# Kernel tuning notes

Hardware: AMD Instinct MI355X
Metric: run time of the kernel (lower is better)

Reference implementation:

```python
import jax, jax.numpy as jnp
import numpy as np

R = 4                 # correlation radius
D = 2 * R + 1         # window size per axis (9)
EPS = 1e-5            # batchnorm eps
DN = ('NCHW', 'OIHW', 'NCHW')


def conv(x, w, stride=1, pad=1):
    return jax.lax.conv_general_dilated(x, w, (stride, stride), [(pad, pad), (pad, pad)], dimension_numbers=DN)


def bn(x, g, b):
    # training-mode batchnorm (batch statistics over N,H,W), matching torch default
    m = jnp.mean(x, axis=(0, 2, 3), keepdims=True)
    v = jnp.var(x, axis=(0, 2, 3), keepdims=True)
    return g[None, :, None, None] * (x - m) * jax.lax.rsqrt(v + EPS) + b[None, :, None, None]


def grid_sample(img, grid):
    # bilinear, align_corners=True, zero padding; img (B,C,H,W), grid (B,Ho,Wo,2) in [-1,1]
    B, C, H, W = img.shape
    x = (grid[..., 0] + 1.0) * (W - 1) * 0.5
    y = (grid[..., 1] + 1.0) * (H - 1) * 0.5
    x0 = jnp.floor(x)
    y0 = jnp.floor(y)

    def gather(xi, yi):
        valid = (xi >= 0) & (xi <= W - 1) & (yi >= 0) & (yi <= H - 1)
        xc = jnp.clip(xi, 0, W - 1).astype(jnp.int32)
        yc = jnp.clip(yi, 0, H - 1).astype(jnp.int32)
        v = jax.vmap(lambda im, yy, xx: im[:, yy, xx])(img, yc, xc)  # (B,C,Ho,Wo)
        return v * valid[:, None, :, :].astype(img.dtype)

    wx1 = (x - x0)[:, None]; wx0 = 1.0 - wx1
    wy1 = (y - y0)[:, None]; wy0 = 1.0 - wy1
    return (wy0 * wx0 * gather(x0, y0) + wy0 * wx1 * gather(x0 + 1.0, y0)
            + wy1 * wx0 * gather(x0, y0 + 1.0) + wy1 * wx1 * gather(x0 + 1.0, y0 + 1.0))


def _forward(f1, f2, coords, w1, g1, b1, w2, g2, b2, w3, g3, b3, w4, g4, b4,
             wd, gd, bd, w5, b5, e1w, e1b, e2w, e2b, e3w, e3b, dapw):
    B, C, H, W = f1.shape
    dx = jnp.linspace(-R, R, D)
    delta = jnp.stack(jnp.meshgrid(dx, dx, indexing='ij'), axis=-1)      # (D,D,2)

    # sampling centroids for the (2r+1)^2 displacement window
    cp = coords.transpose(0, 2, 3, 1)                                     # (B,H,W,2)
    cent = cp[:, None, :, None, :, :] + delta.reshape(1, D, 1, D, 1, 2)   # (B,D,H,D,W,2)
    gx = 2.0 * cent[..., 0] / (W - 1) - 1.0
    gy = 2.0 * cent[..., 1] / (H - 1) - 1.0
    grid = jnp.stack([gx, gy], axis=-1).reshape(B, D * H, D * W, 2)

    f2s = grid_sample(f2, grid).reshape(B, C, D, H, D, W).transpose(0, 2, 4, 1, 3, 5)  # (B,D,D,C,H,W)
    f1s = jnp.broadcast_to(f1[:, None, None], (B, D, D, C, H, W))
    ds = jnp.broadcast_to(delta.reshape(1, D, D, 2, 1, 1), (B, D, D, 2, H, W)).astype(f1.dtype)
    stack = jnp.concatenate([f1s, f2s, ds], axis=3).reshape(B * D * D, 2 * C + 2, H, W)

    # MatchingNet (DICL-style): conv/bn/relu with stride-2 down + transposed-conv up
    x = jax.nn.relu(bn(conv(stack, w1), g1, b1))
    x = jax.nn.relu(bn(conv(x, w2, stride=2), g2, b2))
    x = jax.nn.relu(bn(conv(x, w3), g3, b3))
    x = jax.nn.relu(bn(conv(x, w4), g4, b4))
    # ConvTranspose2d(k=4, s=2, p=1) == dilated conv with lhs_dilation=2, pad=k-1-p=2
    x = jax.lax.conv_general_dilated(x, wd, (1, 1), [(2, 2), (2, 2)], lhs_dilation=(2, 2), dimension_numbers=DN)
    x = jax.nn.relu(bn(x, gd, bd))
    cost = (conv(x, w5) + b5[None, :, None, None]).reshape(B, D * D, H, W)

    # PairEmbedding: 1x1-conv MLP on the same stacked volume
    e = jax.nn.relu(conv(stack, e1w, pad=0) + e1b[None, :, None, None])
    e = jax.nn.relu(conv(e, e2w, pad=0) + e2b[None, :, None, None])
    e = (conv(e, e3w, pad=0) + e3b[None, :, None, None]).reshape(B, D * D, -1, H, W)

    # DAP (1x1 conv over displacement channels) + windowed softmax-weighted reduction
    score = jax.nn.softmax(jnp.einsum('od,bdhw->bohw', dapw, cost), axis=1)
    emb = jnp.sum(score[:, :, None] * e, axis=1)                           # (B,emb_dim,H,W)
    return jnp.concatenate([cost, emb], axis=1)                            # (B,81+32,H,W)


def setup_inputs() -> dict:
    keys = iter(jax.random.split(jax.random.key(0), 40))
    B, C, H, W = 2, 32, 64, 64
    cin = 2 * C + 2

    def p(shape, fan):
        return jax.random.normal(next(keys), shape, jnp.float32) * np.float32(np.sqrt(2.0 / fan))

    f1 = jax.random.normal(next(keys), (B, C, H, W), jnp.float32)
    f2 = jax.random.normal(next(keys), (B, C, H, W), jnp.float32)
    yy, xx = jnp.meshgrid(jnp.arange(H, dtype=jnp.float32), jnp.arange(W, dtype=jnp.float32), indexing='ij')
    base = jnp.stack([xx, yy], axis=0)[None]                               # pixel grid (x,y)
    coords = base + 4.0 * jax.random.normal(next(keys), (B, 2, H, W), jnp.float32)

    inp = dict(f1=f1, f2=f2, coords=coords)
    inp.update(w1=p((96, cin, 3, 3), cin * 9), g1=jnp.ones(96), b1=jnp.zeros(96))
    inp.update(w2=p((128, 96, 3, 3), 96 * 9), g2=jnp.ones(128), b2=jnp.zeros(128))
    inp.update(w3=p((128, 128, 3, 3), 128 * 9), g3=jnp.ones(128), b3=jnp.zeros(128))
    inp.update(w4=p((64, 128, 3, 3), 128 * 9), g4=jnp.ones(64), b4=jnp.zeros(64))
    inp.update(wd=p((32, 64, 4, 4), 64 * 16), gd=jnp.ones(32), bd=jnp.zeros(32))
    inp.update(w5=p((1, 32, 3, 3), 32 * 9), b5=jnp.zeros(1))
    inp.update(e1w=p((48, cin, 1, 1), cin), e1b=jnp.zeros(48))
    inp.update(e2w=p((64, 48, 1, 1), 48), e2b=jnp.zeros(64))
    inp.update(e3w=p((32, 64, 1, 1), 64), e3b=jnp.zeros(32))
    inp.update(dapw=jnp.eye(D * D, dtype=jnp.float32))
    return inp


def reference(f1, f2, coords, w1, g1, b1, w2, g2, b2, w3, g3, b3, w4, g4, b4,
              wd, gd, bd, w5, b5, e1w, e1b, e2w, e2b, e3w, e3b, dapw):
    return _forward(f1, f2, coords, w1, g1, b1, w2, g2, b2, w3, g3, b3, w4, g4, b4,
                    wd, gd, bd, w5, b5, e1w, e1b, e2w, e2b, e3w, e3b, dapw)
```

## Files before the change

### kernel.cpp

```cpp
#include <hip/hip_runtime.h>
#include <hip/hip_bf16.h>

typedef _Float16 hf;
typedef short    s8v  __attribute__((ext_vector_type(8)));
typedef _Float16 h8v  __attribute__((ext_vector_type(8)));
typedef float    f32x4 __attribute__((ext_vector_type(4)));

#define DEVINL __device__ __forceinline__

DEVINL unsigned short f2h_bits(float f) { return __builtin_bit_cast(unsigned short, (hf)f); }
DEVINL float h2f_bits(unsigned short u) { return (float)__builtin_bit_cast(hf, u); }

static constexpr size_t OFF_SA    = 0;
static constexpr size_t OFF_F2S   = 524288;
static constexpr size_t OFF_E1    = 42991616;
static constexpr size_t OFF_E2    = 106692608;
static constexpr size_t OFF_E3    = 42991616;
static constexpr size_t OFF_X1    = 85458944;
static constexpr size_t OFF_X2    = 524288;
static constexpr size_t OFF_X3    = 85458944;
static constexpr size_t OFF_X4    = 524288;
static constexpr size_t OFF_XD    = 127926272;
static constexpr size_t OFF_SCORE = 524288;
static constexpr size_t OFF_STATS = 212860928;
static constexpr size_t OFF_WC1   = 212871168;
static constexpr size_t OFF_WC2   = 212981760;
static constexpr size_t OFF_WC3   = 213202944;
static constexpr size_t OFF_WC4   = 213497856;
static constexpr size_t OFF_WDC   = 213645312;
static constexpr size_t OFF_WE1   = 213720064;
static constexpr size_t OFF_WE2   = 213726208;
static constexpr size_t OFF_WE3   = 213734400;
static constexpr size_t OFF_DT1   = 213738496;
static constexpr size_t OFF_DTE   = 213745408;
static constexpr size_t OFF_F2CLF = 213746048;

__global__ void prepack(const float* __restrict__ src, hf* __restrict__ dst,
                        int COr, int COP, int CINr, int CINsrc, int KP, int TAPS) {
  const int idx = blockIdx.x * 256 + threadIdx.x;
  const int total = TAPS * COP * KP;
  if (idx >= total) return;
  const int k = idx % KP;
  const int r = idx / KP;
  const int co = r % COP;
  const int t = r / COP;
  float v = 0.f;
  if (co < COr && k < CINr) v = src[((size_t)co * CINsrc + k) * TAPS + t];
  dst[idx] = (hf)v;
}

__global__ void prepack2(const float* __restrict__ src, hf* __restrict__ dst,
                         int COP, int CIN, int NCHn) {
  const int idx = blockIdx.x * 256 + threadIdx.x;
  const int total = 9 * NCHn * COP * 32;
  if (idx >= total) return;
  const int kk = idx & 31;
  const int r = idx >> 5;
  const int co = r % COP;
  const int r2 = r / COP;
  const int ks = r2 % NCHn;
  const int t = r2 / NCHn;
  dst[idx] = (hf)src[((size_t)co * CIN + ks * 32 + kk) * 9 + t];
}

__global__ void prepack2d(const float* __restrict__ src, hf* __restrict__ dst) {
  const int idx = blockIdx.x * 256 + threadIdx.x;
  if (idx >= 32768) return;
  const int kk = idx & 31;
  const int co = (idx >> 5) & 31;
  const int ks = (idx >> 10) & 1;
  const int tt = (idx >> 11) & 3;
  const int par = idx >> 13;
  const int qq = par >> 1, pp = par & 1;
  const int a = tt >> 1, b = tt & 1;
  dst[idx] = (hf)src[(((size_t)co * 64 + ks * 32 + kk) * 4 + (qq + 2 * a)) * 4 + (pp + 2 * b)];
}

__global__ void dtab1_kernel(const float* __restrict__ w1, float* __restrict__ dtab) {
  const int idx = blockIdx.x * 256 + threadIdx.x;
  if (idx >= 96 * 9 * 2) return;
  const int c = idx & 1;
  const int r = idx >> 1;
  const int pat = r % 9;
  const int co = r / 9;
  const int rc = pat / 3, cc = pat % 3;
  const int kh0 = (rc == 0) ? 1 : 0, kh1 = (rc == 2) ? 1 : 2;
  const int kw0 = (cc == 0) ? 1 : 0, kw1 = (cc == 2) ? 1 : 2;
  float s = 0.f;
  for (int kh = kh0; kh <= kh1; ++kh)
    for (int kw = kw0; kw <= kw1; ++kw)
      s += w1[((size_t)(co * 66 + 64 + c) * 3 + kh) * 3 + kw];
  dtab[(co * 9 + pat) * 2 + c] = s;
}

__global__ void dtabE_kernel(const float* __restrict__ e1w, float* __restrict__ dtE) {
  const int co = threadIdx.x;
  if (co < 48) {
    dtE[co * 2 + 0] = e1w[co * 66 + 64];
    dtE[co * 2 + 1] = e1w[co * 66 + 65];
  }
}

__global__ __launch_bounds__(256) void packf1(const float* __restrict__ f1, hf* __restrict__ sA) {
  const int gid = blockIdx.x * 256 + threadIdx.x;
  const int b = gid >> 12, pix = gid & 4095;
  unsigned words[16];
#pragma unroll
  for (int c = 0; c < 32; c += 2) {
    const float v0 = f1[((size_t)(b * 32 + c)) * 4096 + pix];
    const float v1 = f1[((size_t)(b * 32 + c + 1)) * 4096 + pix];
    words[c >> 1] = (unsigned)f2h_bits(v0) | ((unsigned)f2h_bits(v1) << 16);
  }
  uint4* dst = (uint4*)(sA + (size_t)gid * 32);
#pragma unroll
  for (int i = 0; i < 4; ++i)
    dst[i] = make_uint4(words[4 * i], words[4 * i + 1], words[4 * i + 2], words[4 * i + 3]);
}

__global__ __launch_bounds__(256) void packf2f32(const float* __restrict__ f2,
                                                 float* __restrict__ dst) {
  const int gid = blockIdx.x * 256 + threadIdx.x;
  const int b = gid >> 12, pix = gid & 4095;
  float* op = dst + (size_t)gid * 32;
#pragma unroll
  for (int c = 0; c < 32; c += 4) {
    float4 v;
    v.x = f2[((size_t)(b * 32 + c + 0)) * 4096 + pix];
    v.y = f2[((size_t)(b * 32 + c + 1)) * 4096 + pix];
    v.z = f2[((size_t)(b * 32 + c + 2)) * 4096 + pix];
    v.w = f2[((size_t)(b * 32 + c + 3)) * 4096 + pix];
    *(float4*)(op + c) = v;
  }
}

__global__ __launch_bounds__(256) void sample2(const float* __restrict__ f2clf,
                                               const float* __restrict__ coords,
                                               hf* __restrict__ f2s) {
  const int gid = blockIdx.x * 256 + threadIdx.x;
  const int n = gid >> 12, pix = gid & 4095;
  const int b = n / 81, ij = n - b * 81;
  const float di = (float)(ij / 9) - 4.f, dj = (float)(ij % 9) - 4.f;
  const float x = coords[((size_t)(b * 2 + 0)) * 4096 + pix] + di;
  const float y = coords[((size_t)(b * 2 + 1)) * 4096 + pix] + dj;
  const float x0f = floorf(x), y0f = floorf(y);
  const int x0 = (int)x0f, y0 = (int)y0f;
  const float wx1 = x - x0f, wx0 = 1.f - wx1;
  const float wy1 = y - y0f, wy0 = 1.f - wy1;
  const bool vx0 = (unsigned)x0 < 64u, vx1 = (unsigned)(x0 + 1) < 64u;
  const bool vy0 = (unsigned)y0 < 64u, vy1 = (unsigned)(y0 + 1) < 64u;
  const int x0c = min(max(x0, 0), 63), x1c = min(max(x0 + 1, 0), 63);
  const int y0c = min(max(y0, 0), 63), y1c = min(max(y0 + 1, 0), 63);
  const float w00 = (vy0 && vx0) ? wy0 * wx0 : 0.f;
  const float w01 = (vy0 && vx1) ? wy0 * wx1 : 0.f;
  const float w10 = (vy1 && vx0) ? wy1 * wx0 : 0.f;
  const float w11 = (vy1 && vx1) ? wy1 * wx1 : 0.f;
  const float* fb = f2clf + (size_t)b * 4096 * 32;
  const float* p00 = fb + (size_t)(y0c * 64 + x0c) * 32;
  const float* p01 = fb + (size_t)(y0c * 64 + x1c) * 32;
  const float* p10 = fb + (size_t)(y1c * 64 + x0c) * 32;
  const float* p11 = fb + (size_t)(y1c * 64 + x1c) * 32;
  unsigned words[16];
#pragma unroll
  for (int ch = 0; ch < 16; ++ch) {
    const float2 a  = *(const float2*)(p00 + ch * 2);
    const float2 bb = *(const float2*)(p01 + ch * 2);
    const float2 c  = *(const float2*)(p10 + ch * 2);
    const float2 d  = *(const float2*)(p11 + ch * 2);
    const float v0 = w00 * a.x + w01 * bb.x + w10 * c.x + w11 * d.x;
    const float v1 = w00 * a.y + w01 * bb.y + w10 * c.y + w11 * d.y;
    words[ch] = (unsigned)f2h_bits(v0) | ((unsigned)f2h_bits(v1) << 16);
  }
  uint4* dst = (uint4*)(f2s + (size_t)gid * 32);
#pragma unroll
  for (int i = 0; i < 4; ++i)
    dst[i] = make_uint4(words[4 * i], words[4 * i + 1], words[4 * i + 2], words[4 * i + 3]);
}

DEVINL s8v bnin_apply(s8v v, const float* bnst, int gci) {
  const f32x4 scA = *(const f32x4*)(bnst + 256 + gci);
  const f32x4 scB = *(const f32x4*)(bnst + 256 + gci + 4);
  const f32x4 shA = *(const f32x4*)(bnst + 384 + gci);
  const f32x4 shB = *(const f32x4*)(bnst + 384 + gci + 4);
  h8v h = __builtin_bit_cast(h8v, v);
#pragma unroll
  for (int jj = 0; jj < 8; ++jj) {
    const float sc = (jj < 4) ? scA[jj] : scB[jj - 4];
    const float sh = (jj < 4) ? shA[jj] : shB[jj - 4];
    h[jj] = (hf)fmaxf((float)h[jj] * sc + sh, 0.f);
// ... 58 lines not shown
          const int gci = k0 + lg * 8;
          if (gci < G)
            bfr = *(const h8v*)(src1 + (((size_t)n * NPIXI + pix) * G + gci));
        }
#pragma unroll
        for (int mf = 0; mf < MFR; ++mf)
          acc[mf][pf] = __builtin_amdgcn_mfma_f32_16x16x32_f16(afr[mf], bfr, acc[mf][pf], 0, 0, 0);
      }
    }
  } else {
    s8v rbuf[CPT];
    auto stage_load = [&](int k0) {
#pragma unroll
      for (int j = 0; j < CPT; ++j) {
        const int cidx = tid + j * 256;
        s8v v = (s8v){0, 0, 0, 0, 0, 0, 0, 0};
        if (cidx < NCHUNK) {
          const int s = cidx >> 2, p = cidx & 3;
          const int rs = s / TC, cs = s - rs * TC;
          int ir, ic;
          if (GEOM == 1) { ir = 2 * r0 - 1 + rs; ic = (cs < 32) ? 2 * cs : 2 * (cs - 32) - 1; }
          else           { ir = r0 - 1 + rs;     ic = cs - 1; }
          const int gci = k0 + p * 8;
          if (((unsigned)ir < (unsigned)IMGI) && ((unsigned)ic < (unsigned)IMGI)) {
            const int ipix = ir * IMGI + ic;
            if (DUAL) {
              if (gci < 32)
                v = *(const s8v*)(src0 + (((size_t)b * NPIXI + ipix) * 32 + gci));
              else
                v = *(const s8v*)(src1 + (((size_t)n * NPIXI + ipix) * 32 + (gci - 32)));
            } else if (gci < G) {
              v = *(const s8v*)(src1 + (((size_t)n * NPIXI + ipix) * G + gci));
              if constexpr (BNIN) v = bnin_apply(v, bnst, gci);
            }
          }
        }
        rbuf[j] = v;
      }
    };
    auto stage_write = [&]() {
#pragma unroll
      for (int j = 0; j < CPT; ++j) {
        const int cidx = tid + j * 256;
        if (cidx < NCHUNK) {
          const int s = cidx >> 2, p = cidx & 3;
          *(s8v*)(&lds[(size_t)(p * PSTR + s) * 8]) = rbuf[j];
        }
      }
    };

    stage_load(0);
#pragma unroll
    for (int ch = 0; ch < NCH; ++ch) {
      if (ch > 0) __syncthreads();
      stage_write();
      __syncthreads();
      if (ch + 1 < NCH) stage_load((ch + 1) * 32);
      const int k0 = ch * 32;
#pragma unroll
      for (int t = 0; t < TAPS; ++t) {
        int dh, dw, wt, kh = 0, kw = 0;
        if (GEOM == 2) {
          dh = qq + (t >> 1) - 1; dw = pp + (t & 1) - 1;
          wt = (qq + 2 * (t >> 1)) * 4 + (pp + 2 * (t & 1));
        } else { kh = t / 3; kw = t % 3; dh = kh - 1; dw = kw - 1; wt = t; }
        h8v afr[MFR];
#pragma unroll
        for (int mf = 0; mf < MFR; ++mf)
          afr[mf] = *(const h8v*)(wp + ((size_t)(wt * COP + co0 + mf * 16 + ln)) * KP + k0 + lg * 8);
#pragma unroll
        for (int pf = 0; pf < WPIX; ++pf) {
          const int pl = wid * (WPIX * 16) + pf * 16 + ln;
          const int rL = pl / IMGO, c = pl - rL * IMGO;
          int slot;
          if (GEOM == 1) slot = (2 * rL + kh) * 65 + ((kw == 1) ? c : (32 + c + (kw >> 1)));
          else           slot = (rL + dh + 1) * TC + (c + dw + 1);
          const h8v bfr = *(const h8v*)(&lds[(size_t)(lg * PSTR + slot) * 8]);
#pragma unroll
          for (int mf = 0; mf < MFR; ++mf)
            acc[mf][pf] = __builtin_amdgcn_mfma_f32_16x16x32_f16(afr[mf], bfr, acc[mf][pf], 0, 0, 0);
        }
      }
    }
  }

  const float di = (float)(ij / 9) - 4.f, dj = (float)(ij % 9) - 4.f;

  {
#pragma unroll
    for (int mf = 0; mf < MFR; ++mf) {
#pragma unroll
      for (int pf = 0; pf < WPIX; ++pf) {
        const int pl = wid * (WPIX * 16) + pf * 16 + ln;
        const int rL = pl / IMGO, c = pl - rL * IMGO;
        int opix;
        if constexpr (GEOM == 2) opix = (2 * (r0 + rL) + qq) * 64 + 2 * c + pp;
        else opix = (r0 + rL) * IMGO + c;
        if constexpr (DELTA && EPI == 0) {
          const int oh = r0 + rL;
          const int rc = (oh == 0) ? 0 : ((oh == IMGO - 1) ? 2 : 1);
          const int cc = (c == 0) ? 0 : ((c == IMGO - 1) ? 2 : 1);
#pragma unroll
          for (int rg = 0; rg < 4; ++rg) {
            const int co = co0 + mf * 16 + lg * 4 + rg;
            acc[mf][pf][rg] += di * dtab[(co * 9 + rc * 3 + cc) * 2 + 0] +
                               dj * dtab[(co * 9 + rc * 3 + cc) * 2 + 1];
          }
        }
        if constexpr (DELTA && EPI == 1) {
#pragma unroll
          for (int rg = 0; rg < 4; ++rg) {
            const int co = co0 + mf * 16 + lg * 4 + rg;
            acc[mf][pf][rg] += di * dtab[co * 2] + dj * dtab[co * 2 + 1];
          }
        }
        if constexpr (EPI == 1 || EPI == 2) {
          const float4 bv = *(const float4*)(bias + co0 + mf * 16 + lg * 4);
          acc[mf][pf][0] += bv.x; acc[mf][pf][1] += bv.y;
          acc[mf][pf][2] += bv.z; acc[mf][pf][3] += bv.w;
          if constexpr (EPI == 1) {
#pragma unroll
            for (int rg = 0; rg < 4; ++rg) acc[mf][pf][rg] = fmaxf(acc[mf][pf][rg], 0.f);
          }
        }
        ushort4 st;
        st.x = f2h_bits(acc[mf][pf][0]); st.y = f2h_bits(acc[mf][pf][1]);
        st.z = f2h_bits(acc[mf][pf][2]); st.w = f2h_bits(acc[mf][pf][3]);
        *reinterpret_cast<ushort4*>(outB + ((size_t)n * NPIXO + opix) * COB + co0 + mf * 16 + lg * 4) = st;
      }
    }
    if constexpr (EPI == 0) {
      __syncthreads();
      float* sl = (float*)lds;
#pragma unroll
      for (int mf = 0; mf < MFR; ++mf) {
#pragma unroll
        for (int rg = 0; rg < 4; ++rg) {
          float s = 0.f, q2 = 0.f;
#pragma unroll
          for (int pf = 0; pf < WPIX; ++pf) {
            const float v = acc[mf][pf][rg];
            s += v; q2 += v * v;
          }
#pragma unroll
          for (int o = 1; o < 16; o <<= 1) { s += __shfl_xor(s, o); q2 += __shfl_xor(q2, o); }
          if (ln == 0) {
            const int cl = mf * 16 + lg * 4 + rg;
            sl[(wid * MFR * 16 + cl) * 2 + 0] = s;
            sl[(wid * MFR * 16 + cl) * 2 + 1] = q2;
          }
        }
      }
      __syncthreads();
      for (int i = tid; i < MFR * 16 * 2; i += 256) {
        const int cl = i >> 1, stt = i & 1;
        float tot = 0.f;
#pragma unroll
        for (int w = 0; w < 4; ++w) tot += sl[(w * MFR * 16 + cl) * 2 + stt];
        atomicAdd(&statL[2 * (co0 + cl) + stt], tot);
      }
    }
  }
  (void)outF;
}

__global__ __launch_bounds__(256) void mconv2s2(
    const hf* __restrict__ src1, const hf* __restrict__ wp,
    const float* __restrict__ bnst, float* __restrict__ statL, hf* __restrict__ outB) {
  constexpr int IMGI = 64, IMGO = 32;
  constexpr int PIXROWS = 4, WPIX = 2, MFR = 4;
  constexpr int TR = 2 * PIXROWS + 1;
  constexpr int TC = 65;
  constexpr int NSLOT = TR * TC;
  constexpr int PSTR = NSLOT + 1;
  constexpr int NCH = 3;
  constexpr int G = 96;
  constexpr int NPIXI = IMGI * IMGI;
  constexpr int NCHUNK = NSLOT * 4;
  constexpr int COT = MFR * 16;
  constexpr int COP = 128;
  constexpr int WPLANE = 3 * COT;
  constexpr int WPSTR  = WPLANE + 1;
  constexpr int WCHUNK = WPLANE * 4;

  __shared__ __align__(16) hf alds[4 * PSTR * 8];
  __shared__ __align__(16) hf wlds[4 * WPSTR * 8];

  const int tid = threadIdx.x;
  const int wid = tid >> 6, lane = tid & 63, lg = lane >> 4, ln = lane & 15;
  const int n = blockIdx.z;
  const int r0 = blockIdx.x * PIXROWS;
  const int co0 = (int)blockIdx.y * COT;

  f32x4 acc[MFR][WPIX];
#pragma unroll
  for (int mf = 0; mf < MFR; ++mf)
#pragma unroll
    for (int pf = 0; pf < WPIX; ++pf) acc[mf][pf] = (f32x4){0.f, 0.f, 0.f, 0.f};

  for (int ks = 0; ks < NCH; ++ks) {
    const int k0 = ks * 32;
    __syncthreads();
    for (int cidx = tid; cidx < NCHUNK; cidx += 256) {
      const int s = cidx >> 2, p = cidx & 3;
      const int rs = s / TC, cs = s - rs * TC;
      const int ir = 2 * r0 - 1 + rs;
      const int ic = (cs < 32) ? 2 * cs : 2 * (cs - 32) - 1;
      s8v v = (s8v){0, 0, 0, 0, 0, 0, 0, 0};
      const int gci = k0 + p * 8;
      if (((unsigned)ir < (unsigned)IMGI) && ((unsigned)ic < (unsigned)IMGI)) {
        const int ipix = ir * IMGI + ic;
        v = *(const s8v*)(src1 + (((size_t)n * NPIXI + ipix) * G + gci));
        v = bnin_apply(v, bnst, gci);
      }
      *(s8v*)(&alds[(size_t)(p * PSTR + s) * 8]) = v;
    }
#pragma unroll
    for (int tg = 0; tg < 3; ++tg) {
      if (tg > 0) __syncthreads();
      for (int widx = tid; widx < WCHUNK; widx += 256) {
        const int p = widx & 3;
        const int r = widx >> 2;
        const int co = r & (COT - 1);
        const int tt = r >> 6;
        const int tglob = tg * 3 + tt;
        const s8v wv = *(const s8v*)(wp + (((size_t)(tglob * NCH + ks) * COP + co0 + co) * 32 + p * 8));
        *(s8v*)(&wlds[(size_t)(p * WPSTR + r) * 8]) = wv;
      }
      __syncthreads();
#pragma unroll
      for (int tt = 0; tt < 3; ++tt) {
        const int kh = tg, kw = tt;
        h8v afr[MFR];
#pragma unroll
        for (int mf = 0; mf < MFR; ++mf)
          afr[mf] = *(const h8v*)(&wlds[(size_t)(lg * WPSTR + tt * COT + mf * 16 + ln) * 8]);
#pragma unroll
        for (int pf = 0; pf < WPIX; ++pf) {
          const int pl = wid * (WPIX * 16) + pf * 16 + ln;
          const int rL = pl / IMGO, c = pl - rL * IMGO;
          const int slot = (2 * rL + kh) * 65 + ((kw == 1) ? c : (32 + c + (kw >> 1)));
          const h8v bfr = *(const h8v*)(&alds[(size_t)(lg * PSTR + slot) * 8]);
#pragma unroll
          for (int mf = 0; mf < MFR; ++mf)
            acc[mf][pf] = __builtin_amdgcn_mfma_f32_16x16x32_f16(afr[mf], bfr, acc[mf][pf], 0, 0, 0);
        }
      }
    }
  }

#pragma unroll
  for (int mf = 0; mf < MFR; ++mf) {
#pragma unroll
    for (int pf = 0; pf < WPIX; ++pf) {
      const int pl = wid * (WPIX * 16) + pf * 16 + ln;
      const int rL = pl / IMGO, c = pl - rL * IMGO;
      const int opix = (r0 + rL) * IMGO + c;
      ushort4 st;
      st.x = f2h_bits(acc[mf][pf][0]); st.y = f2h_bits(acc[mf][pf][1]);
      st.z = f2h_bits(acc[mf][pf][2]); st.w = f2h_bits(acc[mf][pf][3]);
      *reinterpret_cast<ushort4*>(outB + ((size_t)n * 1024 + opix) * COP + co0 + mf * 16 + lg * 4) = st;
    }
  }
  __syncthreads();
  float* sl = (float*)alds;
#pragma unroll
  for (int mf = 0; mf < MFR; ++mf) {
#pragma unroll
    for (int rg = 0; rg < 4; ++rg) {
      float s = 0.f, q2 = 0.f;
#pragma unroll
      for (int pf = 0; pf < WPIX; ++pf) {
        const float v = acc[mf][pf][rg];
        s += v; q2 += v * v;
      }
#pragma unroll
      for (int o = 1; o < 16; o <<= 1) { s += __shfl_xor(s, o); q2 += __shfl_xor(q2, o); }
      if (ln == 0) {
        const int cl = mf * 16 + lg * 4 + rg;
        sl[(wid * MFR * 16 + cl) * 2 + 0] = s;
        sl[(wid * MFR * 16 + cl) * 2 + 1] = q2;
      }
    }
  }
  __syncthreads();
  for (int i = tid; i < MFR * 16 * 2; i += 256) {
    const int cl = i >> 1, stt = i & 1;
    float tot = 0.f;
#pragma unroll
    for (int w = 0; w < 4; ++w) tot += sl[(w * MFR * 16 + cl) * 2 + stt];
    atomicAdd(&statL[2 * (co0 + cl) + stt], tot);
  }
}

template <int G, int COP, int MFR, int PIXROWS, int WPIX, bool BNIN>
__global__ __launch_bounds__(256) void mconv2(
    const hf* __restrict__ src1, const hf* __restrict__ wp,
    const float* __restrict__ bnst,
    float* __restrict__ statL, hf* __restrict__ outB) {
  constexpr int IMG = 32;
  constexpr int TAPS = 9;
  constexpr int TC = IMG + 2;
  constexpr int TR = PIXROWS + 2;
  constexpr int NSLOT = TR * TC;
  constexpr int PSTR = NSLOT + 1;
  constexpr int NCH = G / 32;
  constexpr int NPIX = IMG * IMG;
  constexpr int NCHUNK = NSLOT * 4;
  constexpr int COT = MFR * 16;
  constexpr int WPLANE = TAPS * COT;
  constexpr int WPSTR  = WPLANE + 1;
  constexpr int WCHUNK = WPLANE * 4;

  __shared__ __align__(16) hf alds[4 * PSTR * 8];
  __shared__ __align__(16) hf wlds[4 * WPSTR * 8];

  const int tid = threadIdx.x;
  const int wid = tid >> 6, lane = tid & 63, lg = lane >> 4, ln = lane & 15;
  const int n = blockIdx.z;
  const int r0 = blockIdx.x * PIXROWS;
  const int co0 = blockIdx.y * COT;

  f32x4 acc[MFR][WPIX];
#pragma unroll
  for (int mf = 0; mf < MFR; ++mf)
#pragma unroll
    for (int pf = 0; pf < WPIX; ++pf) acc[mf][pf] = (f32x4){0.f, 0.f, 0.f, 0.f};

  for (int ks = 0; ks < NCH; ++ks) {
    __syncthreads();
    for (int cidx = tid; cidx < NCHUNK; cidx += 256) {
      const int s = cidx >> 2, p = cidx & 3;
      const int rs = s / TC, cs = s - rs * TC;
      const int ir = r0 - 1 + rs, ic = cs - 1;
      s8v v = (s8v){0, 0, 0, 0, 0, 0, 0, 0};
      if (((unsigned)ir < (unsigned)IMG) && ((unsigned)ic < (unsigned)IMG)) {
        const int ipix = ir * IMG + ic;
        v = *(const s8v*)(src1 + (((size_t)n * NPIX + ipix) * G + ks * 32 + p * 8));
        if constexpr (BNIN) v = bnin_apply(v, bnst, ks * 32 + p * 8);
      }
      *(s8v*)(&alds[(size_t)(p * PSTR + s) * 8]) = v;
    }
    for (int widx = tid; widx < WCHUNK; widx += 256) {
      const int p = widx & 3;
      const int r = widx >> 2;
      const int co = r & (COT - 1);
      const int t = r >> 6;
      const s8v wv = *(const s8v*)(wp + (((size_t)(t * NCH + ks) * COP + co0 + co) * 32 + p * 8));
      *(s8v*)(&wlds[(size_t)(p * WPSTR + r) * 8]) = wv;
    }
    __syncthreads();
#pragma unroll
    for (int t = 0; t < TAPS; ++t) {
      const int kh = t / 3, kw = t % 3;
      const int dh = kh - 1, dw = kw - 1;
      h8v afr[MFR];
#pragma unroll
      for (int mf = 0; mf < MFR; ++mf)
        afr[mf] = *(const h8v*)(&wlds[(size_t)(lg * WPSTR + t * COT + mf * 16 + ln) * 8]);
#pragma unroll
      for (int pf = 0; pf < WPIX; ++pf) {
        const int pl = wid * (WPIX * 16) + pf * 16 + ln;
        const int rL = pl / IMG, c = pl - rL * IMG;
        const int slot = (rL + dh + 1) * TC + (c + dw + 1);
        const h8v bfr = *(const h8v*)(&alds[(size_t)(lg * PSTR + slot) * 8]);
#pragma unroll
        for (int mf = 0; mf < MFR; ++mf)
          acc[mf][pf] = __builtin_amdgcn_mfma_f32_16x16x32_f16(afr[mf], bfr, acc[mf][pf], 0, 0, 0);
      }
    }
  }

#pragma unroll
  for (int mf = 0; mf < MFR; ++mf) {
#pragma unroll
    for (int pf = 0; pf < WPIX; ++pf) {
      const int pl = wid * (WPIX * 16) + pf * 16 + ln;
      const int rL = pl / IMG, c = pl - rL * IMG;
      const int opix = (r0 + rL) * IMG + c;
      ushort4 st;
      st.x = f2h_bits(acc[mf][pf][0]); st.y = f2h_bits(acc[mf][pf][1]);
      st.z = f2h_bits(acc[mf][pf][2]); st.w = f2h_bits(acc[mf][pf][3]);
      *reinterpret_cast<ushort4*>(outB + ((size_t)n * NPIX + opix) * COP + co0 + mf * 16 + lg * 4) = st;
    }
  }
  __syncthreads();
  float* sl = (float*)alds;
#pragma unroll
  for (int mf = 0; mf < MFR; ++mf) {
#pragma unroll
    for (int rg = 0; rg < 4; ++rg) {
      float s = 0.f, q2 = 0.f;
#pragma unroll
      for (int pf = 0; pf < WPIX; ++pf) {
        const float v = acc[mf][pf][rg];
        s += v; q2 += v * v;
      }
#pragma unroll
      for (int o = 1; o < 16; o <<= 1) { s += __shfl_xor(s, o); q2 += __shfl_xor(q2, o); }
      if (ln == 0) {
        const int cl = mf * 16 + lg * 4 + rg;
        sl[(wid * MFR * 16 + cl) * 2 + 0] = s;
        sl[(wid * MFR * 16 + cl) * 2 + 1] = q2;
      }
    }
  }
  __syncthreads();
  for (int i = tid; i < MFR * 16 * 2; i += 256) {
    const int cl = i >> 1, stt = i & 1;
    float tot = 0.f;
#pragma unroll
    for (int w = 0; w < 4; ++w) tot += sl[(w * MFR * 16 + cl) * 2 + stt];
    atomicAdd(&statL[2 * (co0 + cl) + stt], tot);
  }
}

__global__ __launch_bounds__(256) void mconv2d(
    const hf* __restrict__ src1, const hf* __restrict__ wp,
    const float* __restrict__ bnst,
    float* __restrict__ statL, hf* __restrict__ outB) {
  constexpr int IMG = 32;
  constexpr int TAPS = 4;
  constexpr int PIXROWS = 8;
  constexpr int WPIX = 4;
  constexpr int MFR = 2;
  constexpr int TC = IMG + 2;
  constexpr int TR = PIXROWS + 2;
  constexpr int NSLOT = TR * TC;
  constexpr int PSTR = NSLOT + 1;
  constexpr int NCH = 2;
  constexpr int NPIX = IMG * IMG;
  constexpr int NCHUNK = NSLOT * 4;
  constexpr int COT = MFR * 16;
  constexpr int WPLANE = TAPS * COT;
  constexpr int WPSTR  = WPLANE + 1;
  constexpr int WCHUNK = WPLANE * 4;
  constexpr int G = 64;

  __shared__ __align__(16) hf alds[4 * PSTR * 8];
  __shared__ __align__(16) hf wlds[4 * WPSTR * 8];

  const int tid = threadIdx.x;
  const int wid = tid >> 6, lane = tid & 63, lg = lane >> 4, ln = lane & 15;
  const int n = blockIdx.z;
  const int r0 = blockIdx.x * PIXROWS;
  const int par = blockIdx.y;
  const int qq = par >> 1, pp = par & 1;
  const hf* wbase = wp + (size_t)par * (TAPS * NCH * COT * 32);

  f32x4 acc[MFR][WPIX];
#pragma unroll
  for (int mf = 0; mf < MFR; ++mf)
#pragma unroll
    for (int pf = 0; pf < WPIX; ++pf) acc[mf][pf] = (f32x4){0.f, 0.f, 0.f, 0.f};

  for (int ks = 0; ks < NCH; ++ks) {
    __syncthreads();
    const int k0 = ks * 32;
    for (int cidx = tid; cidx < NCHUNK; cidx += 256) {
      const int s = cidx >> 2, p = cidx & 3;
      const int rs = s / TC, cs = s - rs * TC;
      const int ir = r0 - 1 + rs, ic = cs - 1;
      s8v v = (s8v){0, 0, 0, 0, 0, 0, 0, 0};
      if (((unsigned)ir < (unsigned)IMG) && ((unsigned)ic < (unsigned)IMG)) {
        const int ipix = ir * IMG + ic;
        v = *(const s8v*)(src1 + (((size_t)n * NPIX + ipix) * G + k0 + p * 8));
        v = bnin_apply(v, bnst, k0 + p * 8);
      }
      *(s8v*)(&alds[(size_t)(p * PSTR + s) * 8]) = v;
    }
    for (int widx = tid; widx < WCHUNK; widx += 256) {
      const int p = widx & 3;
      const int r = widx >> 2;
      const int co = r & (COT - 1);
      const int t = r >> 5;
      const s8v wv = *(const s8v*)(wbase + (((size_t)(t * NCH + ks) * COT + co) * 32 + p * 8));
      *(s8v*)(&wlds[(size_t)(p * WPSTR + r) * 8]) = wv;
    }
    __syncthreads();
#pragma unroll
    for (int t = 0; t < TAPS; ++t) {
      const int dh = qq + (t >> 1) - 1;
      const int dw = pp + (t & 1) - 1;
      h8v afr[MFR];
#pragma unroll
      for (int mf = 0; mf < MFR; ++mf)
        afr[mf] = *(const h8v*)(&wlds[(size_t)(lg * WPSTR + t * COT + mf * 16 + ln) * 8]);
#pragma unroll
      for (int pf = 0; pf < WPIX; ++pf) {
        const int pl = wid * (WPIX * 16) + pf * 16 + ln;
        const int rL = pl / IMG, c = pl - rL * IMG;
        const int slot = (rL + dh + 1) * TC + (c + dw + 1);
        const h8v bfr = *(const h8v*)(&alds[(size_t)(lg * PSTR + slot) * 8]);
#pragma unroll
        for (int mf = 0; mf < MFR; ++mf)
          acc[mf][pf] = __builtin_amdgcn_mfma_f32_16x16x32_f16(afr[mf], bfr, acc[mf][pf], 0, 0, 0);
      }
    }
  }

#pragma unroll
  for (int mf = 0; mf < MFR; ++mf) {
#pragma unroll
    for (int pf = 0; pf < WPIX; ++pf) {
      const int pl = wid * (WPIX * 16) + pf * 16 + ln;
      const int rL = pl / IMG, c = pl - rL * IMG;
      const int opix = (2 * (r0 + rL) + qq) * 64 + 2 * c + pp;
      ushort4 st;
      st.x = f2h_bits(acc[mf][pf][0]); st.y = f2h_bits(acc[mf][pf][1]);
      st.z = f2h_bits(acc[mf][pf][2]); st.w = f2h_bits(acc[mf][pf][3]);
      *reinterpret_cast<ushort4*>(outB + ((size_t)n * 4096 + opix) * 32 + mf * 16 + lg * 4) = st;
    }
  }
  __syncthreads();
  float* sl = (float*)alds;
#pragma unroll
  for (int mf = 0; mf < MFR; ++mf) {
#pragma unroll
    for (int rg = 0; rg < 4; ++rg) {
      float s = 0.f, q2 = 0.f;
#pragma unroll
      for (int pf = 0; pf < WPIX; ++pf) {
        const float v = acc[mf][pf][rg];
        s += v; q2 += v * v;
      }
#pragma unroll
      for (int o = 1; o < 16; o <<= 1) { s += __shfl_xor(s, o); q2 += __shfl_xor(q2, o); }
      if (ln == 0) {
        const int cl = mf * 16 + lg * 4 + rg;
        sl[(wid * MFR * 16 + cl) * 2 + 0] = s;
        sl[(wid * MFR * 16 + cl) * 2 + 1] = q2;
      }
    }
  }
  __syncthreads();
  for (int i = tid; i < MFR * 16 * 2; i += 256) {
    const int cl = i >> 1, stt = i & 1;
    float tot = 0.f;
#pragma unroll
    for (int w = 0; w < 4; ++w) tot += sl[(w * MFR * 16 + cl) * 2 + stt];
    atomicAdd(&statL[2 * cl + stt], tot);
  }
}

__global__ void bnfin_kernel(float* __restrict__ statL, const float* __restrict__ g,
                             const float* __restrict__ bt, int C, float invCnt) {
  const int c = threadIdx.x;
  if (c < C) {
    const float m = statL[2 * c] * invCnt;
    const float var = statL[2 * c + 1] * invCnt - m * m;
    const float sc = g[c] * rsqrtf(var + 1e-5f);
    statL[256 + c] = sc;
    statL[384 + c] = bt[c] - m * sc;
  }
}

__global__ __launch_bounds__(256) void conv5_kernel(
    const hf* __restrict__ xd, const float* __restrict__ w5, const float* __restrict__ b5,
    const float* __restrict__ bnst, float* __restrict__ outp) {
  const int gid = blockIdx.x * 256 + threadIdx.x;
  const int n = gid >> 12, pix = gid & 4095;
  const int b = n / 81, ij = n - b * 81;
  const int oh = pix >> 6, ow = pix & 63;
  float acc = b5[0];
#pragma unroll
  for (int kh = 0; kh < 3; ++kh) {
    const int ih = oh + kh - 1;
#pragma unroll
    for (int kw = 0; kw < 3; ++kw) {
      const int iw = ow + kw - 1;
      if (((unsigned)ih < 64u) && ((unsigned)iw < 64u)) {
        const hf* xp = xd + ((size_t)n * 4096 + ih * 64 + iw) * 32;
#pragma unroll
        for (int cq = 0; cq < 4; ++cq) {
          const h8v v = *(const h8v*)(xp + cq * 8);
#pragma unroll
          for (int j = 0; j < 8; ++j) {
            const int c = cq * 8 + j;
            const float t = (hf)fmaxf((float)v[j] * bnst[256 + c] + bnst[384 + c], 0.f);
            acc += t * w5[c * 9 + kh * 3 + kw];
          }
        }
      }
    }
  }
  outp[((size_t)(b * 113 + ij)) * 4096 + pix] = acc;
}

__global__ __launch_bounds__(64) void softmax_kernel(
    const float* __restrict__ outp, const float* __restrict__ dapw, float* __restrict__ score) {
  __shared__ float cb[64 * 81];
  __shared__ float sb[64 * 81];
  const int t = threadIdx.x;
  const int gid = blockIdx.x * 64 + t;
  const int b = gid >> 12, hw = gid & 4095;
  for (int d = 0; d < 81; ++d)
    cb[t * 81 + d] = outp[((size_t)(b * 113 + d)) * 4096 + hw];
  float smax = -1e30f;
  for (int o = 0; o < 81; ++o) {
    float s = 0.f;
    const float* dr = dapw + o * 81;
    for (int d = 0; d < 81; ++d) s += dr[d] * cb[t * 81 + d];
    sb[t * 81 + o] = s;
    smax = fmaxf(smax, s);
  }
  float sum = 0.f;
  for (int o = 0; o < 81; ++o) {
    const float e = __expf(sb[t * 81 + o] - smax);
    sb[t * 81 + o] = e;
    sum += e;
  }
  const float inv = 1.f / sum;
  for (int o = 0; o < 81; ++o)
    score[((size_t)(b * 81 + o)) * 4096 + hw] = sb[t * 81 + o] * inv;
}

__global__ __launch_bounds__(256) void emb_kernel(
    const float* __restrict__ score, const hf* __restrict__ e3, float* __restrict__ outp) {
  const int idx = blockIdx.x * 256 + threadIdx.x;
  const int b = idx >> 17, r = idx & 131071, m = r >> 12, hw = r & 4095;
  float acc = 0.f;
  for (int d = 0; d < 81; ++d) {
    const float sc = score[((size_t)(b * 81 + d)) * 4096 + hw];
    acc += sc * (float)e3[(((size_t)(b * 81 + d)) * 4096 + hw) * 32 + m];
  }
  outp[((size_t)(b * 113 + 81 + m)) * 4096 + hw] = acc;
}

extern "C" void kernel_launch(void* const* d_in, const int* in_sizes, int n_in,
                              void* d_out, int out_size, void* d_ws, size_t ws_size,
                              hipStream_t stream) {
  const float* f1     = (const float*)d_in[0];
  const float* f2     = (const float*)d_in[1];
  const float* coords = (const float*)d_in[2];
  const float* w1     = (const float*)d_in[3];
  const float* g1     = (const float*)d_in[4];
  const float* bb1    = (const float*)d_in[5];
  const float* w2     = (const float*)d_in[6];
  const float* g2     = (const float*)d_in[7];
  const float* bb2    = (const float*)d_in[8];
  const float* w3     = (const float*)d_in[9];
  const float* g3     = (const float*)d_in[10];
  const float* bb3    = (const float*)d_in[11];
  const float* w4     = (const float*)d_in[12];
  const float* g4     = (const float*)d_in[13];
  const float* bb4    = (const float*)d_in[14];
  const float* wdcv   = (const float*)d_in[15];
  const float* gd     = (const float*)d_in[16];
  const float* bbd    = (const float*)d_in[17];
  const float* w5     = (const float*)d_in[18];
  const float* b5     = (const float*)d_in[19];
  const float* e1w    = (const float*)d_in[20];
  const float* e1bi   = (const float*)d_in[21];
  const float* e2w    = (const float*)d_in[22];
  const float* e2bi   = (const float*)d_in[23];
  const float* e3w    = (const float*)d_in[24];
  const float* e3bi   = (const float*)d_in[25];
  const float* dapw   = (const float*)d_in[26];
  float* out = (float*)d_out;
  char* ws = (char*)d_ws;

  hf* sA  = (hf*)(ws + OFF_SA);
  hf* f2s = (hf*)(ws + OFF_F2S);
  hf* be1 = (hf*)(ws + OFF_E1);
  hf* be2 = (hf*)(ws + OFF_E2);
  hf* be3 = (hf*)(ws + OFF_E3);
  hf* x1  = (hf*)(ws + OFF_X1);
  hf* x2  = (hf*)(ws + OFF_X2);
  hf* x3  = (hf*)(ws + OFF_X3);
  hf* x4  = (hf*)(ws + OFF_X4);
  hf* xd  = (hf*)(ws + OFF_XD);
  float* score = (float*)(ws + OFF_SCORE);
  float* stats = (float*)(ws + OFF_STATS);
  hf* wc1 = (hf*)(ws + OFF_WC1);
  hf* wc2 = (hf*)(ws + OFF_WC2);
  hf* wc3 = (hf*)(ws + OFF_WC3);
  hf* wc4 = (hf*)(ws + OFF_WC4);
  hf* wdc = (hf*)(ws + OFF_WDC);
  hf* we1 = (hf*)(ws + OFF_WE1);
  hf* we2 = (hf*)(ws + OFF_WE2);
  hf* we3 = (hf*)(ws + OFF_WE3);
  float* dt1 = (float*)(ws + OFF_DT1);
  float* dtE = (float*)(ws + OFF_DTE);
  float* f2clf = (float*)(ws + OFF_F2CLF);

  hipMemsetAsync(stats, 0, 2560 * sizeof(float), stream);

  prepack<<<216, 256, 0, stream>>>(w1,   wc1, 96, 96, 64, 66, 64, 9);
  prepack2<<<432, 256, 0, stream>>>(w2,  wc2, 128, 96, 3);
  prepack2<<<576, 256, 0, stream>>>(w3,  wc3, 128, 128, 4);
  prepack2<<<288, 256, 0, stream>>>(w4,  wc4, 64, 128, 4);
  prepack2d<<<128, 256, 0, stream>>>(wdcv, wdc);
  prepack<<<12,  256, 0, stream>>>(e1w,  we1, 48, 48, 64, 66, 64, 1);
  prepack<<<16,  256, 0, stream>>>(e2w,  we2, 64, 64, 48, 48, 64, 1);
  prepack<<<8,   256, 0, stream>>>(e3w,  we3, 32, 32, 64, 64, 64, 1);
  dtab1_kernel<<<7, 256, 0, stream>>>(w1, dt1);
  dtabE_kernel<<<1, 96, 0, stream>>>(e1w, dtE);

  packf1<<<32, 256, 0, stream>>>(f1, sA);
  packf2f32<<<32, 256, 0, stream>>>(f2, f2clf);
  sample2<<<2592, 256, 0, stream>>>(f2clf, coords, f2s);

  mconv<3, 1, true, false, 32, 64, 48, 48, 3, 64, 64, 4, 4, true>
      <<<dim3(16, 1, 162), 256, 0, stream>>>(f2s, sA, we1, e1bi, dtE, nullptr, nullptr, be1, nullptr);
  mconv<3, 1, false, false, 48, 64, 64, 64, 4, 64, 64, 4, 4, false>
      <<<dim3(16, 1, 162), 256, 0, stream>>>(be1, nullptr, we2, e2bi, nullptr, nullptr, nullptr, be2, nullptr);
  mconv<3, 2, false, false, 64, 64, 32, 32, 2, 64, 64, 4, 4, false>
      <<<dim3(16, 1, 162), 256, 0, stream>>>(be2, nullptr, we3, e3bi, nullptr, nullptr, nullptr, be3, nullptr);

  mconv<0, 0, true, false, 32, 64, 96, 96, 3, 64, 64, 4, 4, true>
      <<<dim3(16, 2, 162), 256, 0, stream>>>(f2s, sA, wc1, nullptr, dt1, stats + 0, nullptr, x1, nullptr);
  bnfin_kernel<<<1, 128, 0, stream>>>(stats + 0, g1, bb1, 96, 1.f / 663552.f);

  mconv2s2<<<dim3(8, 2, 162), 256, 0, stream>>>(x1, wc2, stats + 0, stats + 512, x2);
  bnfin_kernel<<<1, 128, 0, stream>>>(stats + 512, g2, bb2, 128, 1.f / 165888.f);

  mconv2<128, 128, 4, 4, 2, true>
      <<<dim3(8, 2, 162), 256, 0, stream>>>(x2, wc3, stats + 512, stats + 1024, x3);
  bnfin_kernel<<<1, 128, 0, stream>>>(stats + 1024, g3, bb3, 128, 1.f / 165888.f);

  mconv2<128, 64, 4, 4, 2, true>
      <<<dim3(8, 1, 162), 256, 0, stream>>>(x3, wc4, stats + 1024, stats + 1536, x4);
  bnfin_kernel<<<1, 128, 0, stream>>>(stats + 1536, g4, bb4, 64, 1.f / 165888.f);

  mconv2d<<<dim3(4, 4, 162), 256, 0, stream>>>(x4, wdc, stats + 1536, stats + 2048, xd);
  bnfin_kernel<<<1, 128, 0, stream>>>(stats + 2048, gd, bbd, 32, 1.f / 663552.f);

  conv5_kernel<<<2592, 256, 0, stream>>>(xd, w5, b5, stats + 2048, out);

  softmax_kernel<<<128, 64, 0, stream>>>(out, dapw, score);
  emb_kernel<<<1024, 256, 0, stream>>>(score, be3, out);

  (void)in_sizes; (void)n_in; (void)out_size; (void)ws_size;
}
```

Measured before the change: 924.9 us.

## Fuse embedding 1x1 conv chain and replace BN-stat atomics with partial-sum reduction

Three 1x1 embedding conv kernels become one kernel that keeps the intermediate activations in LDS, so the be1/be2 buffers no longer go through global memory. BatchNorm statistics are no longer accumulated with float atomicAdd. Each block writes its partial sums to a per-block slot, a new bnred kernel reduces them in double precision, and bnfin computes scale and shift in double. This removes atomic contention and the extra round trips to global memory, at the cost of a few more small launches, and it also changes numerical precision and determinism.

```diff
diff --git a/kernel.cpp b/kernel.cpp
--- a/kernel.cpp
+++ b/kernel.cpp
@@ -13,8 +13,6 @@
 
 static constexpr size_t OFF_SA    = 0;
 static constexpr size_t OFF_F2S   = 524288;
-static constexpr size_t OFF_E1    = 42991616;
-static constexpr size_t OFF_E2    = 106692608;
 static constexpr size_t OFF_E3    = 42991616;
 static constexpr size_t OFF_X1    = 85458944;
 static constexpr size_t OFF_X2    = 524288;
@@ -34,6 +32,8 @@
 static constexpr size_t OFF_DT1   = 213738496;
 static constexpr size_t OFF_DTE   = 213745408;
 static constexpr size_t OFF_F2CLF = 213746048;
+static constexpr size_t OFF_PART  = 214794752;
+static constexpr size_t OFF_STATD = 216785920;
 
 __global__ void prepack(const float* __restrict__ src, hf* __restrict__ dst,
                         int COr, int COP, int CINr, int CINsrc, int KP, int TAPS) {
@@ -398,16 +398,158 @@
         }
       }
       __syncthreads();
+      const int NPB = gridDim.x * gridDim.z;
+      const int pb = (int)blockIdx.x * gridDim.z + blockIdx.z;
       for (int i = tid; i < MFR * 16 * 2; i += 256) {
         const int cl = i >> 1, stt = i & 1;
         float tot = 0.f;
 #pragma unroll
         for (int w = 0; w < 4; ++w) tot += sl[(w * MFR * 16 + cl) * 2 + stt];
-        atomicAdd(&statL[2 * (co0 + cl) + stt], tot);
+        statL[(size_t)((co0 + cl) * 2 + stt) * NPB + pb] = tot;
       }
     }
   }
   (void)outF;
+}
+
+__global__ __launch_bounds__(256) void efuse(
+    const hf* __restrict__ f2s_, const hf* __restrict__ sA_,
+    const hf* __restrict__ w1p, const float* __restrict__ b1v, const float* __restrict__ dtE,
+    const hf* __restrict__ w2p, const float* __restrict__ b2v,
+    const hf* __restrict__ w3p, const float* __restrict__ b3v,
+    hf* __restrict__ outB) {
+  constexpr int PSTRE = 72;
+  __shared__ __align__(16) hf ldsA[256 * PSTRE];
+  __shared__ __align__(16) hf ldsB[256 * PSTRE];
+
+  const int tid = threadIdx.x;
+  const int wid = tid >> 6, lane = tid & 63, lg = lane >> 4, ln = lane & 15;
+  const int n = blockIdx.z, b = n / 81, ij = n - b * 81;
+  const int r0 = blockIdx.x * 4;
+  const float di = (float)(ij / 9) - 4.f, dj = (float)(ij % 9) - 4.f;
+
+  f32x4 acc1[3][4];
+#pragma unroll
+  for (int mf = 0; mf < 3; ++mf)
+#pragma unroll
+    for (int pf = 0; pf < 4; ++pf) acc1[mf][pf] = (f32x4){0.f, 0.f, 0.f, 0.f};
+#pragma unroll
+  for (int ch = 0; ch < 2; ++ch) {
+    const int k0 = ch * 32;
+    h8v afr[3];
+#pragma unroll
+    for (int mf = 0; mf < 3; ++mf)
+      afr[mf] = *(const h8v*)(w1p + ((size_t)(mf * 16 + ln)) * 64 + k0 + lg * 8);
+#pragma unroll
+    for (int pf = 0; pf < 4; ++pf) {
+      const int pix = r0 * 64 + wid * 64 + pf * 16 + ln;
+      const h8v bfr = (ch == 0)
+          ? *(const h8v*)(sA_ + (((size_t)b * 4096 + pix) * 32 + lg * 8))
+          : *(const h8v*)(f2s_ + (((size_t)n * 4096 + pix) * 32 + lg * 8));
+#pragma unroll
+      for (int mf = 0; mf < 3; ++mf)
+        acc1[mf][pf] = __builtin_amdgcn_mfma_f32_16x16x32_f16(afr[mf], bfr, acc1[mf][pf], 0, 0, 0);
+    }
+  }
+#pragma unroll
+  for (int mf = 0; mf < 3; ++mf) {
+#pragma unroll
+    for (int pf = 0; pf < 4; ++pf) {
+      const int pixL = wid * 64 + pf * 16 + ln;
+#pragma unroll
+      for (int rg = 0; rg < 4; ++rg) {
+        const int co = mf * 16 + lg * 4 + rg;
+        acc1[mf][pf][rg] += di * dtE[co * 2] + dj * dtE[co * 2 + 1];
+      }
+      const float4 bv = *(const float4*)(b1v + mf * 16 + lg * 4);
+      acc1[mf][pf][0] += bv.x; acc1[mf][pf][1] += bv.y;
+      acc1[mf][pf][2] += bv.z; acc1[mf][pf][3] += bv.w;
+#pragma unroll
+      for (int rg = 0; rg < 4; ++rg) acc1[mf][pf][rg] = fmaxf(acc1[mf][pf][rg], 0.f);
+      ushort4 st;
+      st.x = f2h_bits(acc1[mf][pf][0]); st.y = f2h_bits(acc1[mf][pf][1]);
+      st.z = f2h_bits(acc1[mf][pf][2]); st.w = f2h_bits(acc1[mf][pf][3]);
+      *reinterpret_cast<ushort4*>(&ldsA[(size_t)pixL * PSTRE + mf * 16 + lg * 4]) = st;
+    }
+  }
+  for (int z = tid; z < 256 * 16; z += 256)
+    ldsA[(size_t)(z >> 4) * PSTRE + 48 + (z & 15)] = (hf)0.f;
+  __syncthreads();
+
+  f32x4 acc2[4][4];
+#pragma unroll
+  for (int mf = 0; mf < 4; ++mf)
+#pragma unroll
+    for (int pf = 0; pf < 4; ++pf) acc2[mf][pf] = (f32x4){0.f, 0.f, 0.f, 0.f};
+#pragma unroll
+  for (int ch = 0; ch < 2; ++ch) {
+    const int k0 = ch * 32;
+    h8v afr[4];
+#pragma unroll
+    for (int mf = 0; mf < 4; ++mf)
+      afr[mf] = *(const h8v*)(w2p + ((size_t)(mf * 16 + ln)) * 64 + k0 + lg * 8);
+#pragma unroll
+    for (int pf = 0; pf < 4; ++pf) {
+      const int pixL = wid * 64 + pf * 16 + ln;
+      const h8v bfr = *(const h8v*)(&ldsA[(size_t)pixL * PSTRE + k0 + lg * 8]);
+#pragma unroll
+      for (int mf = 0; mf < 4; ++mf)
+        acc2[mf][pf] = __builtin_amdgcn_mfma_f32_16x16x32_f16(afr[mf], bfr, acc2[mf][pf], 0, 0, 0);
+    }
+  }
+#pragma unroll
+  for (int mf = 0; mf < 4; ++mf) {
+#pragma unroll
+    for (int pf = 0; pf < 4; ++pf) {
+      const int pixL = wid * 64 + pf * 16 + ln;
+      const float4 bv = *(const float4*)(b2v + mf * 16 + lg * 4);
+      acc2[mf][pf][0] += bv.x; acc2[mf][pf][1] += bv.y;
+      acc2[mf][pf][2] += bv.z; acc2[mf][pf][3] += bv.w;
+#pragma unroll
+      for (int rg = 0; rg < 4; ++rg) acc2[mf][pf][rg] = fmaxf(acc2[mf][pf][rg], 0.f);
+      ushort4 st;
+      st.x = f2h_bits(acc2[mf][pf][0]); st.y = f2h_bits(acc2[mf][pf][1]);
+      st.z = f2h_bits(acc2[mf][pf][2]); st.w = f2h_bits(acc2[mf][pf][3]);
+      *reinterpret_cast<ushort4*>(&ldsB[(size_t)pixL * PSTRE + mf * 16 + lg * 4]) = st;
+    }
+  }
+  __syncthreads();
+
+  f32x4 acc3[2][4];
+#pragma unroll
+  for (int mf = 0; mf < 2; ++mf)
+#pragma unroll
+    for (int pf = 0; pf < 4; ++pf) acc3[mf][pf] = (f32x4){0.f, 0.f, 0.f, 0.f};
+#pragma unroll
+  for (int ch = 0; ch < 2; ++ch) {
+    const int k0 = ch * 32;
+    h8v afr[2];
+#pragma unroll
+    for (int mf = 0; mf < 2; ++mf)
+      afr[mf] = *(const h8v*)(w3p + ((size_t)(mf * 16 + ln)) * 64 + k0 + lg * 8);
+#pragma unroll
+    for (int pf = 0; pf < 4; ++pf) {
+      const int pixL = wid * 64 + pf * 16 + ln;
+      const h8v bfr = *(const h8v*)(&ldsB[(size_t)pixL * PSTRE + k0 + lg * 8]);
+#pragma unroll
+      for (int mf = 0; mf < 2; ++mf)
+        acc3[mf][pf] = __builtin_amdgcn_mfma_f32_16x16x32_f16(afr[mf], bfr, acc3[mf][pf], 0, 0, 0);
+    }
+  }
+#pragma unroll
+  for (int mf = 0; mf < 2; ++mf) {
+#pragma unroll
+    for (int pf = 0; pf < 4; ++pf) {
+      const int pix = r0 * 64 + wid * 64 + pf * 16 + ln;
+      const float4 bv = *(const float4*)(b3v + mf * 16 + lg * 4);
+      acc3[mf][pf][0] += bv.x; acc3[mf][pf][1] += bv.y;
+      acc3[mf][pf][2] += bv.z; acc3[mf][pf][3] += bv.w;
+      ushort4 st;
+      st.x = f2h_bits(acc3[mf][pf][0]); st.y = f2h_bits(acc3[mf][pf][1]);
+      st.z = f2h_bits(acc3[mf][pf][2]); st.w = f2h_bits(acc3[mf][pf][3]);
+      *reinterpret_cast<ushort4*>(outB + (((size_t)n * 4096 + pix) * 32 + mf * 16 + lg * 4)) = st;
+    }
+  }
 }
 
 __global__ __launch_bounds__(256) void mconv2s2(
@@ -530,12 +672,14 @@
     }
   }
   __syncthreads();
+  const int NPB = gridDim.x * gridDim.z;
+  const int pb = (int)blockIdx.x * gridDim.z + blockIdx.z;
   for (int i = tid; i < MFR * 16 * 2; i += 256) {
     const int cl = i >> 1, stt = i & 1;
     float tot = 0.f;
 #pragma unroll
     for (int w = 0; w < 4; ++w) tot += sl[(w * MFR * 16 + cl) * 2 + stt];
-    atomicAdd(&statL[2 * (co0 + cl) + stt], tot);
+    statL[(size_t)((co0 + cl) * 2 + stt) * NPB + pb] = tot;
   }
 }
 
@@ -652,12 +796,14 @@
     }
   }
   __syncthreads();
+  const int NPB = gridDim.x * gridDim.z;
+  const int pb = (int)blockIdx.x * gridDim.z + blockIdx.z;
   for (int i = tid; i < MFR * 16 * 2; i += 256) {
     const int cl = i >> 1, stt = i & 1;
     float tot = 0.f;
 #pragma unroll
     for (int w = 0; w < 4; ++w) tot += sl[(w * MFR * 16 + cl) * 2 + stt];
-    atomicAdd(&statL[2 * (co0 + cl) + stt], tot);
+    statL[(size_t)((co0 + cl) * 2 + stt) * NPB + pb] = tot;
   }
 }
 
@@ -780,24 +926,41 @@
     }
   }
   __syncthreads();
+  const int NPB = gridDim.x * gridDim.y * gridDim.z;
+  const int pb = ((int)blockIdx.y * gridDim.x + blockIdx.x) * gridDim.z + blockIdx.z;
   for (int i = tid; i < MFR * 16 * 2; i += 256) {
     const int cl = i >> 1, stt = i & 1;
     float tot = 0.f;
 #pragma unroll
     for (int w = 0; w < 4; ++w) tot += sl[(w * MFR * 16 + cl) * 2 + stt];
-    atomicAdd(&statL[2 * cl + stt], tot);
-  }
-}
-
-__global__ void bnfin_kernel(float* __restrict__ statL, const float* __restrict__ g,
-                             const float* __restrict__ bt, int C, float invCnt) {
+    statL[(size_t)(cl * 2 + stt) * NPB + pb] = tot;
+  }
+}
+
+__global__ __launch_bounds__(256) void bnred(const float* __restrict__ part,
+                                             double* __restrict__ statD, int NPB) {
+  const int chstat = blockIdx.x;
+  const int t = threadIdx.x;
+  double s = 0.0;
+  for (int p = t; p < NPB; p += 256) s += (double)part[(size_t)chstat * NPB + p];
+#pragma unroll
+  for (int o = 1; o < 64; o <<= 1) s += __shfl_xor(s, o);
+  __shared__ double wsum[4];
+  if ((t & 63) == 0) wsum[t >> 6] = s;
+  __syncthreads();
+  if (t == 0) statD[chstat] = (wsum[0] + wsum[1]) + (wsum[2] + wsum[3]);
+}
+
+__global__ void bnfin_kernel(const double* __restrict__ statD, float* __restrict__ statL,
+                             const float* __restrict__ g, const float* __restrict__ bt,
+                             int C, double invCnt) {
   const int c = threadIdx.x;
   if (c < C) {
-    const float m = statL[2 * c] * invCnt;
-    const float var = statL[2 * c + 1] * invCnt - m * m;
-    const float sc = g[c] * rsqrtf(var + 1e-5f);
-    statL[256 + c] = sc;
-    statL[384 + c] = bt[c] - m * sc;
+    const double m = statD[2 * c] * invCnt;
+    const double var = statD[2 * c + 1] * invCnt - m * m;
+    const double sc = (double)g[c] / sqrt(var + 1e-5);
+    statL[256 + c] = (float)sc;
+    statL[384 + c] = (float)((double)bt[c] - m * sc);
   }
 }
 
@@ -908,8 +1071,6 @@
 
   hf* sA  = (hf*)(ws + OFF_SA);
   hf* f2s = (hf*)(ws + OFF_F2S);
-  hf* be1 = (hf*)(ws + OFF_E1);
-  hf* be2 = (hf*)(ws + OFF_E2);
   hf* be3 = (hf*)(ws + OFF_E3);
   hf* x1  = (hf*)(ws + OFF_X1);
   hf* x2  = (hf*)(ws + OFF_X2);
@@ -929,6 +1090,8 @@
   float* dt1 = (float*)(ws + OFF_DT1);
   float* dtE = (float*)(ws + OFF_DTE);
   float* f2clf = (float*)(ws + OFF_F2CLF);
+  float* part = (float*)(ws + OFF_PART);
+  double* statD = (double*)(ws + OFF_STATD);
 
   hipMemsetAsync(stats, 0, 2560 * sizeof(float), stream);
 
@@ -947,30 +1110,30 @@
   packf2f32<<<32, 256, 0, stream>>>(f2, f2clf);
   sample2<<<2592, 256, 0, stream>>>(f2clf, coords, f2s);
 
-  mconv<3, 1, true, false, 32, 64, 48, 48, 3, 64, 64, 4, 4, true>
-      <<<dim3(16, 1, 162), 256, 0, stream>>>(f2s, sA, we1, e1bi, dtE, nullptr, nullptr, be1, nullptr);
-  mconv<3, 1, false, false, 48, 64, 64, 64, 4, 64, 64, 4, 4, false>
-      <<<dim3(16, 1, 162), 256, 0, stream>>>(be1, nullptr, we2, e2bi, nullptr, nullptr, nullptr, be2, nullptr);
-  mconv<3, 2, false, false, 64, 64, 32, 32, 2, 64, 64, 4, 4, false>
-      <<<dim3(16, 1, 162), 256, 0, stream>>>(be2, nullptr, we3, e3bi, nullptr, nullptr, nullptr, be3, nullptr);
+  efuse<<<dim3(16, 1, 162), 256, 0, stream>>>(f2s, sA, we1, e1bi, dtE, we2, e2bi, we3, e3bi, be3);
 
   mconv<0, 0, true, false, 32, 64, 96, 96, 3, 64, 64, 4, 4, true>
-      <<<dim3(16, 2, 162), 256, 0, stream>>>(f2s, sA, wc1, nullptr, dt1, stats + 0, nullptr, x1, nullptr);
-  bnfin_kernel<<<1, 128, 0, stream>>>(stats + 0, g1, bb1, 96, 1.f / 663552.f);
-
-  mconv2s2<<<dim3(8, 2, 162), 256, 0, stream>>>(x1, wc2, stats + 0, stats + 512, x2);
-  bnfin_kernel<<<1, 128, 0, stream>>>(stats + 512, g2, bb2, 128, 1.f / 165888.f);
+      <<<dim3(16, 2, 162), 256, 0, stream>>>(f2s, sA, wc1, nullptr, dt1, part, nullptr, x1, nullptr);
+  bnred<<<192, 256, 0, stream>>>(part, statD + 0, 2592);
+  bnfin_kernel<<<1, 128, 0, stream>>>(statD + 0, stats + 0, g1, bb1, 96, 1.0 / 663552.0);
+
+  mconv2s2<<<dim3(8, 2, 162), 256, 0, stream>>>(x1, wc2, stats + 0, part, x2);
+  bnred<<<256, 256, 0, stream>>>(part, statD + 256, 1296);
+  bnfin_kernel<<<1, 128, 0, stream>>>(statD + 256, stats + 512, g2, bb2, 128, 1.0 / 165888.0);
 
   mconv2<128, 128, 4, 4, 2, true>
-      <<<dim3(8, 2, 162), 256, 0, stream>>>(x2, wc3, stats + 512, stats + 1024, x3);
-  bnfin_kernel<<<1, 128, 0, stream>>>(stats + 1024, g3, bb3, 128, 1.f / 165888.f);
+      <<<dim3(8, 2, 162), 256, 0, stream>>>(x2, wc3, stats + 512, part, x3);
+  bnred<<<256, 256, 0, stream>>>(part, statD + 512, 1296);
+  bnfin_kernel<<<1, 128, 0, stream>>>(statD + 512, stats + 1024, g3, bb3, 128, 1.0 / 165888.0);
 
   mconv2<128, 64, 4, 4, 2, true>
-      <<<dim3(8, 1, 162), 256, 0, stream>>>(x3, wc4, stats + 1024, stats + 1536, x4);
-  bnfin_kernel<<<1, 128, 0, stream>>>(stats + 1536, g4, bb4, 64, 1.f / 165888.f);
-
-  mconv2d<<<dim3(4, 4, 162), 256, 0, stream>>>(x4, wdc, stats + 1536, stats + 2048, xd);
-  bnfin_kernel<<<1, 128, 0, stream>>>(stats + 2048, gd, bbd, 32, 1.f / 663552.f);
+      <<<dim3(8, 1, 162), 256, 0, stream>>>(x3, wc4, stats + 1024, part, x4);
+  bnred<<<128, 256, 0, stream>>>(part, statD + 768, 1296);
+  bnfin_kernel<<<1, 128, 0, stream>>>(statD + 768, stats + 1536, g4, bb4, 64, 1.0 / 165888.0);
+
+  mconv2d<<<dim3(4, 4, 162), 256, 0, stream>>>(x4, wdc, stats + 1536, part, xd);
+  bnred<<<64, 256, 0, stream>>>(part, statD + 1024, 2592);
+  bnfin_kernel<<<1, 128, 0, stream>>>(statD + 1024, stats + 2048, gd, bbd, 32, 1.0 / 663552.0);
 
   conv5_kernel<<<2592, 256, 0, stream>>>(xd, w5, b5, stats + 2048, out);
 
```

Result: faster. 798.6 us (-13.7%).
